# Optimization experiments

Hardware: AMD Instinct MI355X
Metric: run time of the kernel (lower is better)

The kernel has to match this reference:

```python
import jax, jax.numpy as jnp
import numpy as np

EMB_DIM = 64
B, S, D = 64, 1024, 64

def setup_inputs() -> dict:
    key = jax.random.key(0)
    k1, k2, k3, k4, k5 = jax.random.split(key, 5)
    return {
        "query": jax.random.normal(k1, (B, S, D), dtype=jnp.float32),
        "key": jax.random.normal(k2, (B, S, D), dtype=jnp.float32),
        "value": jax.random.normal(k3, (B, S, D), dtype=jnp.float32),
        "a_key": jax.random.normal(k4, (S, S, D), dtype=jnp.float32),
        "a_value": jax.random.normal(k5, (S, S, D), dtype=jnp.float32),
    }

def reference(query, key, value, a_key, a_value):
    scale = jnp.sqrt(jnp.asarray(EMB_DIM, dtype=query.dtype))
    # standard content-content scores: [B, Sq, Sk]
    qk = jnp.einsum("bqd,bkd->bqk", query, key)
    # relative key scores: a_key is [Sq, Sk, D]; contract over D per query position
    rel_qk = jnp.einsum("bqd,qkd->bqk", query, a_key)
    attn = jax.nn.softmax((qk + rel_qk) / scale, axis=-1)
    # content values + relative values
    qkv = jnp.einsum("bqk,bkd->bqd", attn, value)
    rel_qkv = jnp.einsum("bqk,qkd->bqd", attn, a_value)
    return qkv + rel_qkv, attn
```

## Files before the change

### kernel.cpp

```cpp
#include <hip/hip_runtime.h>
#include <stdint.h>

#define S_ 1024
#define D_ 64
#define B_ 64

typedef short short8 __attribute__((ext_vector_type(8)));
typedef unsigned short ushort8 __attribute__((ext_vector_type(8)));
typedef float f32x4 __attribute__((ext_vector_type(4)));

__device__ __forceinline__ unsigned short f2bf(float x) {
    uint32_t u = __builtin_bit_cast(uint32_t, x);
    return (unsigned short)((u + 0x7FFFu + ((u >> 16) & 1u)) >> 16);
}
__device__ __forceinline__ float bf2f(unsigned short b) {
    return __builtin_bit_cast(float, ((uint32_t)b) << 16);
}
__device__ __forceinline__ uint32_t pack2(float a, float b) {
    return (uint32_t)f2bf(a) | ((uint32_t)f2bf(b) << 16);
}
__device__ __forceinline__ int scidx(int row, int k) {
    return (((row << 10) + (k & ~7)) ^ ((row & 15) << 3)) + (k & 7);
}

__global__ __launch_bounds__(256) void k1_qk(const float* __restrict__ Q,
                                             const float* __restrict__ Kk,
                                             float* __restrict__ qk) {
    __shared__ __align__(16) unsigned short Qs[128][72];
    __shared__ __align__(16) unsigned short Ks[128][72];
    const float SCL = 0.18033688011112042f;
    const int bx = blockIdx.x;
    const int b  = bx >> 6;
    const int q0 = ((bx >> 3) & 7) << 7;
    const int k0 = (bx & 7) << 7;
    const int t  = threadIdx.x;
#pragma unroll
    for (int i = 0; i < 8; ++i) {
        int f = (i << 8) + t;
        int row = f >> 4, c = (f & 15) << 2;
        float4 v = *reinterpret_cast<const float4*>(&Q[((size_t)(b * S_ + q0 + row) << 6) + c]);
        *reinterpret_cast<uint2*>(&Qs[row][c]) = make_uint2(pack2(v.x, v.y), pack2(v.z, v.w));
        float4 u = *reinterpret_cast<const float4*>(&Kk[((size_t)(b * S_ + k0 + row) << 6) + c]);
        *reinterpret_cast<uint2*>(&Ks[row][c]) = make_uint2(pack2(u.x, u.y), pack2(u.z, u.w));
    }
    __syncthreads();
    const int l = t & 63, w = t >> 6, lr = l & 15, lg = l >> 4;
    short8 a[2][2];
#pragma unroll
    for (int mi = 0; mi < 2; ++mi)
#pragma unroll
        for (int h = 0; h < 2; ++h)
            a[mi][h] = *reinterpret_cast<const short8*>(&Qs[((w * 2 + mi) << 4) + lr][h * 32 + lg * 8]);
    f32x4 acc[2][8] = {};
#pragma unroll
    for (int n = 0; n < 8; ++n) {
        short8 b0 = *reinterpret_cast<const short8*>(&Ks[(n << 4) + lr][lg * 8]);
        short8 b1 = *reinterpret_cast<const short8*>(&Ks[(n << 4) + lr][32 + lg * 8]);
#pragma unroll
        for (int mi = 0; mi < 2; ++mi) {
            acc[mi][n] = __builtin_amdgcn_mfma_f32_16x16x32_bf16(a[mi][0], b0, acc[mi][n], 0, 0, 0);
            acc[mi][n] = __builtin_amdgcn_mfma_f32_16x16x32_bf16(a[mi][1], b1, acc[mi][n], 0, 0, 0);
        }
    }
#pragma unroll
    for (int mi = 0; mi < 2; ++mi)
#pragma unroll
        for (int n = 0; n < 8; ++n)
#pragma unroll
            for (int r = 0; r < 4; ++r) {
                int qq = q0 + ((w * 2 + mi) << 4) + (lg << 2) + r;
                int kc = k0 + (n << 4) + lr;
                qk[((size_t)(b * S_ + qq) << 10) + kc] = acc[mi][n][r] * SCL;
            }
}

__device__ __forceinline__ void tpose_store(unsigned short (*Tls)[72], float4 p,
                                            int kb, int t) {
    const int l = t & 63, lr = l & 15, lg = l >> 4;
    float v0 = p.x, v1 = p.y, v2 = p.z, v3 = p.w;
    float y0 = __shfl_xor(v0, 16), y1 = __shfl_xor(v1, 16),
          y2 = __shfl_xor(v2, 16), y3 = __shfl_xor(v3, 16);
    bool o = (lg & 1);
    float n0 = o ? y1 : v0, n1 = o ? v1 : y0, n2 = o ? y3 : v2, n3 = o ? v3 : y2;
    float z0 = __shfl_xor(n0, 32), z1 = __shfl_xor(n1, 32),
          z2 = __shfl_xor(n2, 32), z3 = __shfl_xor(n3, 32);
    bool h = (lg & 2);
    float T0 = h ? z2 : n0, T1 = h ? z3 : n1, T2 = h ? n2 : z0, T3 = h ? n3 : z1;
    int d = (lr << 2) + lg;
    *reinterpret_cast<uint2*>(&Tls[d][kb]) = make_uint2(pack2(T0, T1), pack2(T2, T3));
}

__global__ __launch_bounds__(512) void k2_mid(const float* __restrict__ Q,
                                              const float* __restrict__ AK,
                                              const float* __restrict__ AV,
                                              float* __restrict__ attn,
                                              float* __restrict__ outp) {
    __shared__ __align__(16) unsigned short Sc[64 * 1024];
    __shared__ __align__(16) unsigned short Qs[64][72];
    __shared__ __align__(16) unsigned short Ak[64][72];
    __shared__ float invs[64];
    const float SCL = 0.18033688011112042f;
    const int q = blockIdx.x;
    const int t = threadIdx.x;
    const int l = t & 63, w = t >> 6, lr = l & 15, lg = l >> 4;
    const int wq = w & 3;
    const int wh = w >> 2;
    const int srow = t >> 3, sc8 = (t & 7) << 3;

    {
        const float* qp = &Q[((size_t)(srow * S_ + q) << 6) + sc8];
        float4 a = *reinterpret_cast<const float4*>(qp);
        float4 b = *reinterpret_cast<const float4*>(qp + 4);
        *reinterpret_cast<uint4*>(&Qs[srow][sc8]) =
            make_uint4(pack2(a.x * SCL, a.y * SCL), pack2(a.z * SCL, a.w * SCL),
                       pack2(b.x * SCL, b.y * SCL), pack2(b.z * SCL, b.w * SCL));
    }
    const float* akbase = &AK[(size_t)q << 16];
    float4 pa0, pa1;
    {
        const float* p_ = akbase + (srow << 6) + sc8;
        pa0 = *reinterpret_cast<const float4*>(p_);
        pa1 = *reinterpret_cast<const float4*>(p_ + 4);
    }
    __syncthreads();
    short8 qa[2][2];
#pragma unroll
    for (int bh = 0; bh < 2; ++bh)
#pragma unroll
        for (int h = 0; h < 2; ++h)
            qa[bh][h] = *reinterpret_cast<const short8*>(
                &Qs[(wh << 5) + (bh << 4) + lr][(h << 5) + (lg << 3)]);

    for (int tt = 0; tt < 16; ++tt) {
        __syncthreads();
        *reinterpret_cast<uint4*>(&Ak[srow][sc8]) =
            make_uint4(pack2(pa0.x, pa0.y), pack2(pa0.z, pa0.w),
                       pack2(pa1.x, pa1.y), pack2(pa1.z, pa1.w));
        __syncthreads();
        if (tt < 15) {
            const float* p_ = akbase + ((size_t)(tt + 1) << 12) + (srow << 6) + sc8;
            pa0 = *reinterpret_cast<const float4*>(p_);
            pa1 = *reinterpret_cast<const float4*>(p_ + 4);
        }
        short8 ak0 = *reinterpret_cast<const short8*>(&Ak[(wq << 4) + lr][lg << 3]);
        short8 ak1 = *reinterpret_cast<const short8*>(&Ak[(wq << 4) + lr][32 + (lg << 3)]);
        int kbase = (tt << 6) + (wq << 4) + (lg << 2);
#pragma unroll
        for (int bh = 0; bh < 2; ++bh) {
            f32x4 c = {};
            c = __builtin_amdgcn_mfma_f32_16x16x32_bf16(ak0, qa[bh][0], c, 0, 0, 0);
            c = __builtin_amdgcn_mfma_f32_16x16x32_bf16(ak1, qa[bh][1], c, 0, 0, 0);
            *reinterpret_cast<uint2*>(&Sc[scidx((wh << 5) + (bh << 4) + lr, kbase)]) =
                make_uint2(pack2(c[0], c[1]), pack2(c[2], c[3]));
        }
    }
    __syncthreads();

    const float* avbase = &AV[(size_t)q << 16];
    float4 pv[2];
#pragma unroll
    for (int i = 0; i < 2; ++i) {
        int f = (i << 9) + t;
        pv[i] = *reinterpret_cast<const float4*>(
            &avbase[((size_t)(f >> 4) << 6) + ((f & 15) << 2)]);
    }

    {
        const int ch = t & 7;
        const float* qkrow = &attn[((size_t)(srow * S_ + q) << 10)];
        float s = 0.f;
#pragma unroll 4
        for (int i = 0; i < 16; ++i) {
            int k = (((i << 3) + ch) << 3);
            float4 g0 = *reinterpret_cast<const float4*>(&qkrow[k]);
            float4 g1 = *reinterpret_cast<const float4*>(&qkrow[k + 4]);
            int idx = scidx(srow, k);
            ushort8 rel = *reinterpret_cast<const ushort8*>(&Sc[idx]);
            float p0 = exp2f(g0.x + bf2f(rel[0]));
            float p1 = exp2f(g0.y + bf2f(rel[1]));
            float p2 = exp2f(g0.z + bf2f(rel[2]));
            float p3 = exp2f(g0.w + bf2f(rel[3]));
            float p4 = exp2f(g1.x + bf2f(rel[4]));
            float p5 = exp2f(g1.y + bf2f(rel[5]));
            float p6 = exp2f(g1.z + bf2f(rel[6]));
            float p7 = exp2f(g1.w + bf2f(rel[7]));
            s += ((p0 + p1) + (p2 + p3)) + ((p4 + p5) + (p6 + p7));
            ushort8 e;
            e[0] = f2bf(p0); e[1] = f2bf(p1); e[2] = f2bf(p2); e[3] = f2bf(p3);
            e[4] = f2bf(p4); e[5] = f2bf(p5); e[6] = f2bf(p6); e[7] = f2bf(p7);
            *reinterpret_cast<ushort8*>(&Sc[idx]) = e;
        }
        s += __shfl_xor(s, 1); s += __shfl_xor(s, 2); s += __shfl_xor(s, 4);
        if (ch == 0) invs[srow] = 1.0f / s;
    }
    __syncthreads();

    f32x4 oacc[2] = {};
    for (int tt = 0; tt < 16; ++tt) {
        __syncthreads();
        tpose_store(Ak, pv[0], (w << 2), t);
        tpose_store(Ak, pv[1], 32 + (w << 2), t);
        __syncthreads();
        if (tt < 15) {
#pragma unroll
            for (int i = 0; i < 2; ++i) {
                int f = (i << 9) + t;
                pv[i] = *reinterpret_cast<const float4*>(
                    &avbase[((size_t)(tt + 1) << 12) + ((size_t)(f >> 4) << 6) + ((f & 15) << 2)]);
            }
        }
        {
            int col = (t & 255) << 2;
#pragma unroll
            for (int rr = 0; rr < 2; ++rr) {
                int row = (tt << 2) + (rr << 1) + wh;
                uint2 u = *reinterpret_cast<const uint2*>(&Sc[scidx(row, col)]);
                float inv = invs[row];
                float4 o = make_float4(bf2f((unsigned short)(u.x & 0xffff)) * inv,
                                       bf2f((unsigned short)(u.x >> 16)) * inv,
                                       bf2f((unsigned short)(u.y & 0xffff)) * inv,
                                       bf2f((unsigned short)(u.y >> 16)) * inv);
                *reinterpret_cast<float4*>(&attn[((size_t)(row * S_ + q) << 10) + col]) = o;
            }
        }
        short8 bb0 = *reinterpret_cast<const short8*>(&Ak[(wq << 4) + lr][lg << 3]);
        short8 bb1 = *reinterpret_cast<const short8*>(&Ak[(wq << 4) + lr][32 + (lg << 3)]);
#pragma unroll
        for (int mi = 0; mi < 2; ++mi) {
            short8 ea0 = *reinterpret_cast<const short8*>(
                &Sc[scidx((wh << 5) + (mi << 4) + lr, (tt << 6) + (lg << 3))]);
            short8 ea1 = *reinterpret_cast<const short8*>(
                &Sc[scidx((wh << 5) + (mi << 4) + lr, (tt << 6) + 32 + (lg << 3))]);
            oacc[mi] = __builtin_amdgcn_mfma_f32_16x16x32_bf16(ea0, bb0, oacc[mi], 0, 0, 0);
            oacc[mi] = __builtin_amdgcn_mfma_f32_16x16x32_bf16(ea1, bb1, oacc[mi], 0, 0, 0);
        }
    }
#pragma unroll
    for (int mi = 0; mi < 2; ++mi)
#pragma unroll
        for (int r = 0; r < 4; ++r) {
            int brow = (wh << 5) + (mi << 4) + (lg << 2) + r;
            outp[((size_t)(brow * S_ + q) << 6) + (wq << 4) + lr] = oacc[mi][r] * invs[brow];
        }
}

__global__ __launch_bounds__(256) void k3_pv(const float* __restrict__ V,
                                             const float* __restrict__ attn,
                                             float* __restrict__ outp) {
    __shared__ __align__(16) unsigned short At[64][72];
    __shared__ __align__(16) unsigned short Vt[64][72];
    const int b  = blockIdx.x >> 4;
    const int q0 = (blockIdx.x & 15) << 6;
    const int t  = threadIdx.x;
    const int l = t & 63, w = t >> 6, lr = l & 15, lg = l >> 4;
    float4 pa[4], pv[4];
#pragma unroll
    for (int i = 0; i < 4; ++i) {
        int f = (i << 8) + t;
        int row = f >> 4, c = (f & 15) << 2;
        pa[i] = *reinterpret_cast<const float4*>(&attn[((size_t)(b * S_ + q0 + row) << 10) + c]);
        pv[i] = *reinterpret_cast<const float4*>(&V[((size_t)(b * S_ + row) << 6) + c]);
    }
    f32x4 acc[4] = {};
    for (int tt = 0; tt < 16; ++tt) {
        __syncthreads();
#pragma unroll
        for (int i = 0; i < 4; ++i) {
            int f = (i << 8) + t;
            int row = f >> 4, c = (f & 15) << 2;
            *reinterpret_cast<uint2*>(&At[row][c]) =
                make_uint2(pack2(pa[i].x, pa[i].y), pack2(pa[i].z, pa[i].w));
            tpose_store(Vt, pv[i], (i << 4) + (w << 2), t);
        }
        __syncthreads();
        if (tt < 15) {
#pragma unroll
            for (int i = 0; i < 4; ++i) {
                int f = (i << 8) + t;
                int row = f >> 4, c = (f & 15) << 2;
                pa[i] = *reinterpret_cast<const float4*>(
                    &attn[((size_t)(b * S_ + q0 + row) << 10) + ((tt + 1) << 6) + c]);
                pv[i] = *reinterpret_cast<const float4*>(
                    &V[((size_t)(b * S_ + ((tt + 1) << 6) + row) << 6) + c]);
            }
        }
        short8 a0 = *reinterpret_cast<const short8*>(&At[(w << 4) + lr][lg * 8]);
        short8 a1 = *reinterpret_cast<const short8*>(&At[(w << 4) + lr][32 + lg * 8]);
#pragma unroll
        for (int n = 0; n < 4; ++n) {
            short8 b0 = *reinterpret_cast<const short8*>(&Vt[(n << 4) + lr][lg * 8]);
            short8 b1 = *reinterpret_cast<const short8*>(&Vt[(n << 4) + lr][32 + lg * 8]);
            acc[n] = __builtin_amdgcn_mfma_f32_16x16x32_bf16(a0, b0, acc[n], 0, 0, 0);
            acc[n] = __builtin_amdgcn_mfma_f32_16x16x32_bf16(a1, b1, acc[n], 0, 0, 0);
        }
    }
#pragma unroll
    for (int n = 0; n < 4; ++n)
#pragma unroll
        for (int r = 0; r < 4; ++r) {
            size_t idx = ((size_t)(b * S_ + q0 + (w << 4) + (lg << 2) + r) << 6) + (n << 4) + lr;
            outp[idx] += acc[n][r];
        }
}

extern "C" void kernel_launch(void* const* d_in, const int* in_sizes, int n_in,
                              void* d_out, int out_size, void* d_ws, size_t ws_size,
                              hipStream_t stream) {
    (void)in_sizes; (void)n_in; (void)out_size; (void)d_ws; (void)ws_size;
    const float* Q  = (const float*)d_in[0];
    const float* K  = (const float*)d_in[1];
    const float* V  = (const float*)d_in[2];
    const float* AK = (const float*)d_in[3];
    const float* AV = (const float*)d_in[4];
    float* outp = (float*)d_out;
    float* attn = outp + (size_t)B_ * S_ * D_;

    k1_qk <<<dim3(64 * 8 * 8), dim3(256), 0, stream>>>(Q, K, attn);
    k2_mid<<<dim3(1024),       dim3(512), 0, stream>>>(Q, AK, AV, attn, outp);
    k3_pv <<<dim3(64 * 16),    dim3(256), 0, stream>>>(V, attn, outp);
}
```

Baseline: 407.2 us.

## Double-buffer LDS tiles in k2 and restructure k3 to keep V resident

In k2_mid, the AK and AV tile staging now uses two LDS buffers with loads issued two tiles ahead, so each iteration needs one barrier instead of two. k3_pv is restructured so each 512-thread block transposes the whole V[b] into LDS once, then loops over four 64-row query sub-tiles with double-buffered attention tiles. The grid shrinks from 1024 to 256 blocks. This is meant to cut barrier stalls and avoid reloading V per query tile, at the cost of larger LDS use (about 130KB in k3), higher register pressure and fewer blocks.

```diff
diff --git a/kernel.cpp b/kernel.cpp
--- a/kernel.cpp
+++ b/kernel.cpp
@@ -74,8 +74,8 @@
             }
 }
 
-__device__ __forceinline__ void tpose_store(unsigned short (*Tls)[72], float4 p,
-                                            int kb, int t) {
+__device__ __forceinline__ void tpose_store_p(unsigned short* Tls, int pitch, float4 p,
+                                              int kb, int t) {
     const int l = t & 63, lr = l & 15, lg = l >> 4;
     float v0 = p.x, v1 = p.y, v2 = p.z, v3 = p.w;
     float y0 = __shfl_xor(v0, 16), y1 = __shfl_xor(v1, 16),
@@ -87,7 +87,7 @@
     bool h = (lg & 2);
     float T0 = h ? z2 : n0, T1 = h ? z3 : n1, T2 = h ? n2 : z0, T3 = h ? n3 : z1;
     int d = (lr << 2) + lg;
-    *reinterpret_cast<uint2*>(&Tls[d][kb]) = make_uint2(pack2(T0, T1), pack2(T2, T3));
+    *reinterpret_cast<uint2*>(&Tls[d * pitch + kb]) = make_uint2(pack2(T0, T1), pack2(T2, T3));
 }
 
 __global__ __launch_bounds__(512) void k2_mid(const float* __restrict__ Q,
@@ -97,7 +97,7 @@
                                               float* __restrict__ outp) {
     __shared__ __align__(16) unsigned short Sc[64 * 1024];
     __shared__ __align__(16) unsigned short Qs[64][72];
-    __shared__ __align__(16) unsigned short Ak[64][72];
+    __shared__ __align__(16) unsigned short Ak[2][64][72];
     __shared__ float invs[64];
     const float SCL = 0.18033688011112042f;
     const int q = blockIdx.x;
@@ -116,12 +116,15 @@
                        pack2(b.x * SCL, b.y * SCL), pack2(b.z * SCL, b.w * SCL));
     }
     const float* akbase = &AK[(size_t)q << 16];
-    float4 pa0, pa1;
-    {
-        const float* p_ = akbase + (srow << 6) + sc8;
-        pa0 = *reinterpret_cast<const float4*>(p_);
-        pa1 = *reinterpret_cast<const float4*>(p_ + 4);
-    }
+    float4 pa[2][2];
+#define LDK(set, tile) do { const float* p_ = akbase + ((size_t)(tile) << 12) + (srow << 6) + sc8; \
+        pa[set][0] = *reinterpret_cast<const float4*>(p_);                                         \
+        pa[set][1] = *reinterpret_cast<const float4*>(p_ + 4); } while (0)
+#define STAGEK(buf) do {                                                                     \
+        *reinterpret_cast<uint4*>(&Ak[buf][srow][sc8]) =                                     \
+            make_uint4(pack2(pa[buf][0].x, pa[buf][0].y), pack2(pa[buf][0].z, pa[buf][0].w), \
+                       pack2(pa[buf][1].x, pa[buf][1].y), pack2(pa[buf][1].z, pa[buf][1].w)); } while (0)
+    LDK(0, 0); LDK(1, 1);
     __syncthreads();
     short8 qa[2][2];
 #pragma unroll
@@ -130,20 +133,16 @@
         for (int h = 0; h < 2; ++h)
             qa[bh][h] = *reinterpret_cast<const short8*>(
                 &Qs[(wh << 5) + (bh << 4) + lr][(h << 5) + (lg << 3)]);
-
+    STAGEK(0);
+    __syncthreads();
+
+#pragma unroll 2
     for (int tt = 0; tt < 16; ++tt) {
-        __syncthreads();
-        *reinterpret_cast<uint4*>(&Ak[srow][sc8]) =
-            make_uint4(pack2(pa0.x, pa0.y), pack2(pa0.z, pa0.w),
-                       pack2(pa1.x, pa1.y), pack2(pa1.z, pa1.w));
-        __syncthreads();
-        if (tt < 15) {
-            const float* p_ = akbase + ((size_t)(tt + 1) << 12) + (srow << 6) + sc8;
-            pa0 = *reinterpret_cast<const float4*>(p_);
-            pa1 = *reinterpret_cast<const float4*>(p_ + 4);
-        }
-        short8 ak0 = *reinterpret_cast<const short8*>(&Ak[(wq << 4) + lr][lg << 3]);
-        short8 ak1 = *reinterpret_cast<const short8*>(&Ak[(wq << 4) + lr][32 + (lg << 3)]);
+        const int cur = tt & 1, nxt = cur ^ 1;
+        short8 ak0 = *reinterpret_cast<const short8*>(&Ak[cur][(wq << 4) + lr][lg << 3]);
+        short8 ak1 = *reinterpret_cast<const short8*>(&Ak[cur][(wq << 4) + lr][32 + (lg << 3)]);
+        if (tt < 15) STAGEK(nxt);
+        if (tt < 14) LDK(cur, tt + 2);
         int kbase = (tt << 6) + (wq << 4) + (lg << 2);
 #pragma unroll
         for (int bh = 0; bh < 2; ++bh) {
@@ -153,17 +152,21 @@
             *reinterpret_cast<uint2*>(&Sc[scidx((wh << 5) + (bh << 4) + lr, kbase)]) =
                 make_uint2(pack2(c[0], c[1]), pack2(c[2], c[3]));
         }
-    }
-    __syncthreads();
+        __syncthreads();
+    }
+#undef LDK
+#undef STAGEK
 
     const float* avbase = &AV[(size_t)q << 16];
-    float4 pv[2];
-#pragma unroll
-    for (int i = 0; i < 2; ++i) {
-        int f = (i << 9) + t;
-        pv[i] = *reinterpret_cast<const float4*>(
-            &avbase[((size_t)(f >> 4) << 6) + ((f & 15) << 2)]);
-    }
+    float4 pv[2][2];
+#pragma unroll
+    for (int s = 0; s < 2; ++s)
+#pragma unroll
+        for (int i = 0; i < 2; ++i) {
+            int f = (i << 9) + t;
+            pv[s][i] = *reinterpret_cast<const float4*>(
+                &avbase[((size_t)s << 12) + ((size_t)(f >> 4) << 6) + ((f & 15) << 2)]);
+        }
 
     {
         const int ch = t & 7;
@@ -195,18 +198,26 @@
     }
     __syncthreads();
 
+    tpose_store_p(&Ak[0][0][0], 72, pv[0][0], (w << 2), t);
+    tpose_store_p(&Ak[0][0][0], 72, pv[0][1], 32 + (w << 2), t);
+    __syncthreads();
+
     f32x4 oacc[2] = {};
+#pragma unroll 2
     for (int tt = 0; tt < 16; ++tt) {
-        __syncthreads();
-        tpose_store(Ak, pv[0], (w << 2), t);
-        tpose_store(Ak, pv[1], 32 + (w << 2), t);
-        __syncthreads();
+        const int cur = tt & 1, nxt = cur ^ 1;
+        short8 bb0 = *reinterpret_cast<const short8*>(&Ak[cur][(wq << 4) + lr][lg << 3]);
+        short8 bb1 = *reinterpret_cast<const short8*>(&Ak[cur][(wq << 4) + lr][32 + (lg << 3)]);
         if (tt < 15) {
+            tpose_store_p(&Ak[nxt][0][0], 72, pv[nxt][0], (w << 2), t);
+            tpose_store_p(&Ak[nxt][0][0], 72, pv[nxt][1], 32 + (w << 2), t);
+        }
+        if (tt < 14) {
 #pragma unroll
             for (int i = 0; i < 2; ++i) {
                 int f = (i << 9) + t;
-                pv[i] = *reinterpret_cast<const float4*>(
-                    &avbase[((size_t)(tt + 1) << 12) + ((size_t)(f >> 4) << 6) + ((f & 15) << 2)]);
+                pv[cur][i] = *reinterpret_cast<const float4*>(
+                    &avbase[((size_t)(tt + 2) << 12) + ((size_t)(f >> 4) << 6) + ((f & 15) << 2)]);
             }
         }
         {
@@ -223,8 +234,6 @@
                 *reinterpret_cast<float4*>(&attn[((size_t)(row * S_ + q) << 10) + col]) = o;
             }
         }
-        short8 bb0 = *reinterpret_cast<const short8*>(&Ak[(wq << 4) + lr][lg << 3]);
-        short8 bb1 = *reinterpret_cast<const short8*>(&Ak[(wq << 4) + lr][32 + (lg << 3)]);
 #pragma unroll
         for (int mi = 0; mi < 2; ++mi) {
             short8 ea0 = *reinterpret_cast<const short8*>(
@@ -234,6 +243,7 @@
             oacc[mi] = __builtin_amdgcn_mfma_f32_16x16x32_bf16(ea0, bb0, oacc[mi], 0, 0, 0);
             oacc[mi] = __builtin_amdgcn_mfma_f32_16x16x32_bf16(ea1, bb1, oacc[mi], 0, 0, 0);
         }
+        __syncthreads();
     }
 #pragma unroll
     for (int mi = 0; mi < 2; ++mi)
@@ -244,63 +254,74 @@
         }
 }
 
-__global__ __launch_bounds__(256) void k3_pv(const float* __restrict__ V,
+__global__ __launch_bounds__(512) void k3_pv(const float* __restrict__ V,
                                              const float* __restrict__ attn,
                                              float* __restrict__ outp) {
-    __shared__ __align__(16) unsigned short At[64][72];
-    __shared__ __align__(16) unsigned short Vt[64][72];
-    const int b  = blockIdx.x >> 4;
-    const int q0 = (blockIdx.x & 15) << 6;
+    __shared__ __align__(16) unsigned short Vt[64 * 1032];
+    __shared__ __align__(16) unsigned short At[2][64][72];
+    const int b  = blockIdx.x >> 2;
+    const int qq = blockIdx.x & 3;
     const int t  = threadIdx.x;
     const int l = t & 63, w = t >> 6, lr = l & 15, lg = l >> 4;
-    float4 pa[4], pv[4];
-#pragma unroll
-    for (int i = 0; i < 4; ++i) {
-        int f = (i << 8) + t;
-        int row = f >> 4, c = (f & 15) << 2;
-        pa[i] = *reinterpret_cast<const float4*>(&attn[((size_t)(b * S_ + q0 + row) << 10) + c]);
-        pv[i] = *reinterpret_cast<const float4*>(&V[((size_t)(b * S_ + row) << 6) + c]);
-    }
-    f32x4 acc[4] = {};
-    for (int tt = 0; tt < 16; ++tt) {
+    const int wq = w & 3;
+    const int dh = w >> 2;
+    const int srow = t >> 3, sc8 = (t & 7) << 3;
+
+    for (int kt = 0; kt < 16; ++kt) {
+#pragma unroll
+        for (int i = 0; i < 2; ++i) {
+            int f = (i << 9) + t;
+            int row = f >> 4, c = (f & 15) << 2;
+            float4 pvv = *reinterpret_cast<const float4*>(
+                &V[((size_t)(b * S_ + (kt << 6) + row) << 6) + c]);
+            tpose_store_p(&Vt[0], 1032, pvv, (kt << 6) + (i << 5) + (w << 2), t);
+        }
+    }
+    __syncthreads();
+
+    for (int qs = 0; qs < 4; ++qs) {
+        const float* arow = &attn[((size_t)((b * S_ + (qq << 8) + (qs << 6) + srow)) << 10) + sc8];
+        float4 pa[2][2];
+#define LDA3(set, tile) do { const float* p_ = arow + ((tile) << 6);       \
+        pa[set][0] = *reinterpret_cast<const float4*>(p_);                 \
+        pa[set][1] = *reinterpret_cast<const float4*>(p_ + 4); } while (0)
+#define STAGEA(buf) do {                                                                     \
+        *reinterpret_cast<uint4*>(&At[buf][srow][sc8]) =                                     \
+            make_uint4(pack2(pa[buf][0].x, pa[buf][0].y), pack2(pa[buf][0].z, pa[buf][0].w), \
+                       pack2(pa[buf][1].x, pa[buf][1].y), pack2(pa[buf][1].z, pa[buf][1].w)); } while (0)
+        LDA3(0, 0); LDA3(1, 1);
         __syncthreads();
-#pragma unroll
-        for (int i = 0; i < 4; ++i) {
-            int f = (i << 8) + t;
-            int row = f >> 4, c = (f & 15) << 2;
-            *reinterpret_cast<uint2*>(&At[row][c]) =
-                make_uint2(pack2(pa[i].x, pa[i].y), pack2(pa[i].z, pa[i].w));
-            tpose_store(Vt, pv[i], (i << 4) + (w << 2), t);
-        }
+        STAGEA(0);
         __syncthreads();
-        if (tt < 15) {
-#pragma unroll
-            for (int i = 0; i < 4; ++i) {
-                int f = (i << 8) + t;
-                int row = f >> 4, c = (f & 15) << 2;
-                pa[i] = *reinterpret_cast<const float4*>(
-                    &attn[((size_t)(b * S_ + q0 + row) << 10) + ((tt + 1) << 6) + c]);
-                pv[i] = *reinterpret_cast<const float4*>(
-                    &V[((size_t)(b * S_ + ((tt + 1) << 6) + row) << 6) + c]);
-            }
-        }
-        short8 a0 = *reinterpret_cast<const short8*>(&At[(w << 4) + lr][lg * 8]);
-        short8 a1 = *reinterpret_cast<const short8*>(&At[(w << 4) + lr][32 + lg * 8]);
-#pragma unroll
-        for (int n = 0; n < 4; ++n) {
-            short8 b0 = *reinterpret_cast<const short8*>(&Vt[(n << 4) + lr][lg * 8]);
-            short8 b1 = *reinterpret_cast<const short8*>(&Vt[(n << 4) + lr][32 + lg * 8]);
-            acc[n] = __builtin_amdgcn_mfma_f32_16x16x32_bf16(a0, b0, acc[n], 0, 0, 0);
-            acc[n] = __builtin_amdgcn_mfma_f32_16x16x32_bf16(a1, b1, acc[n], 0, 0, 0);
-        }
-    }
-#pragma unroll
-    for (int n = 0; n < 4; ++n)
-#pragma unroll
-        for (int r = 0; r < 4; ++r) {
-            size_t idx = ((size_t)(b * S_ + q0 + (w << 4) + (lg << 2) + r) << 6) + (n << 4) + lr;
-            outp[idx] += acc[n][r];
-        }
+        f32x4 acc[2] = {};
+#pragma unroll 2
+        for (int kt = 0; kt < 16; ++kt) {
+            const int cur = kt & 1, nxt = cur ^ 1;
+            short8 a0 = *reinterpret_cast<const short8*>(&At[cur][(wq << 4) + lr][lg << 3]);
+            short8 a1 = *reinterpret_cast<const short8*>(&At[cur][(wq << 4) + lr][32 + (lg << 3)]);
+            if (kt < 15) STAGEA(nxt);
+            if (kt < 14) LDA3(cur, kt + 2);
+#pragma unroll
+            for (int n = 0; n < 2; ++n) {
+                const unsigned short* vb = &Vt[((dh << 5) + (n << 4) + lr) * 1032 + (kt << 6) + (lg << 3)];
+                short8 b0 = *reinterpret_cast<const short8*>(vb);
+                short8 b1 = *reinterpret_cast<const short8*>(vb + 32);
+                acc[n] = __builtin_amdgcn_mfma_f32_16x16x32_bf16(a0, b0, acc[n], 0, 0, 0);
+                acc[n] = __builtin_amdgcn_mfma_f32_16x16x32_bf16(a1, b1, acc[n], 0, 0, 0);
+            }
+            __syncthreads();
+        }
+#undef LDA3
+#undef STAGEA
+#pragma unroll
+        for (int n = 0; n < 2; ++n)
+#pragma unroll
+            for (int r = 0; r < 4; ++r) {
+                size_t idx = ((size_t)(b * S_ + (qq << 8) + (qs << 6) + (wq << 4) + (lg << 2) + r) << 6)
+                             + (dh << 5) + (n << 4) + lr;
+                outp[idx] += acc[n][r];
+            }
+    }
 }
 
 extern "C" void kernel_launch(void* const* d_in, const int* in_sizes, int n_in,
@@ -317,5 +338,5 @@
 
     k1_qk <<<dim3(64 * 8 * 8), dim3(256), 0, stream>>>(Q, K, attn);
     k2_mid<<<dim3(1024),       dim3(512), 0, stream>>>(Q, AK, AV, attn, outp);
-    k3_pv <<<dim3(64 * 16),    dim3(256), 0, stream>>>(V, attn, outp);
-}
+    k3_pv <<<dim3(256),        dim3(512), 0, stream>>>(V, attn, outp);
+}
```

Result: no change. 405.6 us (-0.4%).
